# Performance work log

Measured on AMD Instinct MI355X. Metric: run time of the kernel, lower is better.

Reference implementation:

```python
import jax, jax.numpy as jnp
import numpy as np

GRID = 32          # latent grid points per dim
N_OUT = 16384      # output query points
BATCH = 2
C = 256            # projection_channels (latent hidden width)
D = 3              # gno_coord_dim
OUT_CH = 4         # out_channels
RADIUS = 0.045     # gno_radius


def _radius_neighbors(x, y, r):
    """Radius ball search: for each query x_i find all y_j with ||x_i-y_j||<=r.
    Returns (nb_index, out_index) edge lists, sorted by query (CSR order)."""
    r2 = np.float32(r * r)
    nb_idx, out_idx = [], []
    for s in range(0, x.shape[0], 512):  # chunk to bound memory
        d2 = ((x[s:s + 512, None, :] - y[None, :, :]) ** 2).sum(-1)
        oi, yi = np.nonzero(d2 <= r2)
        out_idx.append((oi + s).astype(np.int32))
        nb_idx.append(yi.astype(np.int32))
    return np.concatenate(nb_idx), np.concatenate(out_idx)


def setup_inputs() -> dict:
    key = jax.random.key(0)
    ks = jax.random.split(key, 8)
    # latent queries: regular grid on [0,1]^3
    g = np.linspace(0.0, 1.0, GRID, dtype=np.float32)
    gx, gy, gz = np.meshgrid(g, g, g, indexing="ij")
    grid = np.stack([gx, gy, gz], axis=-1)               # (G,G,G,3)
    latent_queries = jnp.asarray(grid[None])             # (1,G,G,G,3)
    output_queries = jax.random.uniform(ks[0], (1, N_OUT, D), dtype=jnp.float32)
    nb_idx, out_idx = _radius_neighbors(np.asarray(output_queries[0]),
                                        grid.reshape(-1, D), RADIUS)
    latent_embed = jax.random.normal(ks[1], (BATCH, GRID, GRID, GRID, C), dtype=jnp.float32)

    def lin(k, fi, fo):
        kw, kb = jax.random.split(k)
        W = jax.random.normal(kw, (fi, fo), dtype=jnp.float32) / np.sqrt(fi).astype(np.float32)
        b = jax.random.normal(kb, (fo,), dtype=jnp.float32) * 0.01
        return W, b

    W1, b1 = lin(ks[2], 2 * D, 512)
    W2, b2 = lin(ks[3], 512, 256)
    W3, b3 = lin(ks[4], 256, C)
    Wp, bp = lin(ks[5], C, OUT_CH)
    return {"latent_embed": latent_embed, "latent_queries": latent_queries,
            "output_queries": output_queries,
            "nb_index": jnp.asarray(nb_idx), "out_index": jnp.asarray(out_idx),
            "W1": W1, "b1": b1, "W2": W2, "b2": b2, "W3": W3, "b3": b3,
            "Wp": Wp, "bp": bp}


def reference(latent_embed, latent_queries, output_queries, nb_index, out_index,
              W1, b1, W2, b2, W3, b3, Wp, bp):
    y = latent_queries[0].reshape(-1, latent_queries.shape[-1])   # (n_in, d) grid coords
    x = output_queries[0]                                         # (n_out, d)
    n_out = x.shape[0]
    b = latent_embed.shape[0]
    f_y = latent_embed.reshape(b, -1, latent_embed.shape[-1])     # (b, n_in, c)

    # per-edge kernel MLP on concat(y_j, x_i) -- 'linear' transform type
    agg = jnp.concatenate([y[nb_index], x[out_index]], axis=-1)   # (E, 2d)
    h = jax.nn.gelu(agg @ W1 + b1, approximate=False)             # (E, 512)
    h = jax.nn.gelu(h @ W2 + b2, approximate=False)               # (E, 256)
    k = h @ W3 + b3                                               # (E, c) kernel values

    # k(x_i, y_j) * f(y_j), then mean-reduce over each neighborhood
    msg = k[None, :, :] * f_y[:, nb_index, :]                     # (b, E, c)
    sums = jax.vmap(lambda m: jax.ops.segment_sum(m, out_index, num_segments=n_out))(msg)
    cnt = jax.ops.segment_sum(jnp.ones(nb_index.shape[0], dtype=k.dtype),
                              out_index, num_segments=n_out)
    mean = sums / jnp.maximum(cnt, 1.0)[None, :, None]            # (b, n_out, c)

    # pointwise projection (single Linear, no nonlinearity)
    return mean @ Wp + bp                                         # (b, n_out, out_ch)
```

## Files before the change

kernel.cpp:

```cpp
#include <hip/hip_runtime.h>
#include <math.h>

#define NGRID 32768
#define NOUT  16384
#define CCH   256
#define H1DIM 512
#define TE    64
#define NTHR  512

typedef _Float16 f16x8 __attribute__((ext_vector_type(8)));
typedef float    f32x16 __attribute__((ext_vector_type(16)));

#define WAITVM1() asm volatile("s_waitcnt vmcnt(1)" ::: "memory")
#define WAITVM0() asm volatile("s_waitcnt vmcnt(0)" ::: "memory")
#define LGKM0_SB() do { asm volatile("s_waitcnt lgkmcnt(0)" ::: "memory"); \
                        __builtin_amdgcn_sched_barrier(0); } while (0)

typedef const __attribute__((address_space(1))) unsigned int* gas1_t;
typedef __attribute__((address_space(3))) unsigned int* las3_t;

__device__ __forceinline__ void stage16(const void* g, void* l) {
    __builtin_amdgcn_global_load_lds((gas1_t)g, (las3_t)l, 16, 0, 0);
}

__device__ __forceinline__ unsigned short f32_to_f16_bits(float v) {
    _Float16 h = (_Float16)v;
    return __builtin_bit_cast(unsigned short, h);
}

__device__ __forceinline__ float gelu_fast(float x) {
    float ax = fabsf(x) * 0.70710678118654752f;
    float t  = __builtin_amdgcn_rcpf(fmaf(0.3275911f, ax, 1.0f));
    float p  = fmaf(fmaf(fmaf(fmaf(1.061405429f, t, -1.453152027f), t, 1.421413741f), t,
                         -0.284496736f), t, 0.254829592f) * t;
    float e  = __expf(-ax * ax);
    float er = fmaf(-p, e, 1.0f);
    er = (x >= 0.0f) ? er : -er;
    return 0.5f * x * (1.0f + er);
}

__global__ __launch_bounds__(256) void gino_pack_kernel(
    const float* __restrict__ W2, const float* __restrict__ W3,
    unsigned short* __restrict__ W2F, unsigned short* __restrict__ W3F)
{
    int idx = blockIdx.x * 256 + threadIdx.x;
    if (idx < 32 * 8 * 64) {
        int l = idx & 63, g = (idx >> 6) & 7, ks = idx >> 9;
        int ch = g * 32 + (l & 31);
        int k0 = ks * 16 + (l >> 5) * 8;
        unsigned int u[4];
        #pragma unroll
        for (int p = 0; p < 4; ++p) {
            unsigned int lo = f32_to_f16_bits(W2[(k0 + 2 * p) * CCH + ch]);
            unsigned int hh = f32_to_f16_bits(W2[(k0 + 2 * p + 1) * CCH + ch]);
            u[p] = lo | (hh << 16);
        }
        *(uint4*)(W2F + idx * 8) = make_uint4(u[0], u[1], u[2], u[3]);
    } else if (idx < 32 * 8 * 64 + 16 * 8 * 64) {
        int i2 = idx - 32 * 8 * 64;
        int l = i2 & 63, g = (i2 >> 6) & 7, ks = i2 >> 9;
        int ch = g * 32 + (l & 31);
        int k0 = ks * 16 + (l >> 5) * 8;
        unsigned int u[4];
        #pragma unroll
        for (int p = 0; p < 4; ++p) {
            unsigned int lo = f32_to_f16_bits(W3[(k0 + 2 * p) * CCH + ch]);
            unsigned int hh = f32_to_f16_bits(W3[(k0 + 2 * p + 1) * CCH + ch]);
            u[p] = lo | (hh << 16);
        }
        *(uint4*)(W3F + i2 * 8) = make_uint4(u[0], u[1], u[2], u[3]);
    }
}

__global__ __launch_bounds__(NTHR, 4) void gino_edge_kernel(
    const float* __restrict__ latent_embed,
    const float* __restrict__ latent_queries,
    const float* __restrict__ output_queries,
    const int*   __restrict__ nb_index,
    const int*   __restrict__ out_index,
    const float* __restrict__ W1, const float* __restrict__ b1,
    const float* __restrict__ b2, const float* __restrict__ b3,
    const unsigned short* __restrict__ W2F,
    const unsigned short* __restrict__ W3F,
    const float* __restrict__ Wp,
    float* __restrict__ sums, float* __restrict__ cnt, int E)
{
    __shared__ __align__(16) unsigned char s_h1[TE * 256];
    __shared__ __align__(16) unsigned char s_h2[TE * 512];
    __shared__ __align__(16) unsigned char s_ab[8 * 2048];
    __shared__ float s_agg[TE][8];
    __shared__ float s_pm[TE][8];
    __shared__ int s_nb[TE], s_oi[TE], s_valid[TE];

    const int tid = threadIdx.x;
    const int e0  = blockIdx.x * TE;

    ((float*)s_pm)[tid] = 0.0f;
    if (tid < TE) {
        int e     = e0 + tid;
        int valid = (e < E) ? 1 : 0;
        int ec    = valid ? e : (E - 1);
        int nb    = nb_index[ec];
        int oi    = out_index[ec];
        s_nb[tid] = nb; s_oi[tid] = oi; s_valid[tid] = valid;
        s_agg[tid][0] = latent_queries[nb * 3 + 0];
        s_agg[tid][1] = latent_queries[nb * 3 + 1];
        s_agg[tid][2] = latent_queries[nb * 3 + 2];
        s_agg[tid][3] = output_queries[oi * 3 + 0];
        s_agg[tid][4] = output_queries[oi * 3 + 1];
        s_agg[tid][5] = output_queries[oi * 3 + 2];
        if (valid) atomicAdd(&cnt[oi], 1.0f);
    }
    __syncthreads();

    const int l  = tid & 63;
    const int w  = tid >> 6;
    const int le = l & 31;
    const int hi = l >> 5;
    const unsigned bsw1 = (unsigned)(le & 15) << 4;
    const unsigned bsw2 = (unsigned)(le & 31) << 4;
    unsigned char* abw = s_ab + w * 2048;

    f32x16 acc0 = {}, acc1 = {};

    #pragma unroll
    for (int c = 0; c < 4; ++c) {
        const unsigned short* gw = W2F + (size_t)(c * 8) * 4096 + w * 512 + l * 8;
        stage16(gw, abw);
        stage16(gw + 4096, abw + 1024);

        {
            const int col = c * 128 + l * 2;
            float w0[6], w1v[6];
            #pragma unroll
            for (int i = 0; i < 6; ++i) {
                float2 t2 = *(const float2*)(W1 + i * H1DIM + col);
                w0[i] = t2.x; w1v[i] = t2.y;
            }
            float2 bb = *(const float2*)(b1 + col);
            #pragma unroll
            for (int ee = 0; ee < 8; ++ee) {
                int e = w * 8 + ee;
                float v0 = bb.x, v1 = bb.y;
                #pragma unroll
                for (int i = 0; i < 6; ++i) {
                    float a = s_agg[e][i];
                    v0 = fmaf(a, w0[i], v0);
                    v1 = fmaf(a, w1v[i], v1);
                }
                unsigned u = (unsigned)f32_to_f16_bits(gelu_fast(v0)) |
                             ((unsigned)f32_to_f16_bits(gelu_fast(v1)) << 16);
                *(unsigned*)(s_h1 + e * 256 + (((unsigned)(l * 4)) ^ (((unsigned)(e & 15)) << 4))) = u;
            }
        }
        __syncthreads();

        #pragma unroll
        for (int ks = 0; ks < 8; ++ks) {
            if (ks < 7) WAITVM1(); else WAITVM0();
            f16x8 a  = *(const f16x8*)(abw + (ks & 1) * 1024 + l * 16);
            f16x8 b0 = *(const f16x8*)(s_h1 + le * 256 +
                           (((unsigned)(ks * 32 + hi * 16)) ^ bsw1));
            f16x8 b1f = *(const f16x8*)(s_h1 + (32 + le) * 256 +
                           (((unsigned)(ks * 32 + hi * 16)) ^ bsw1));
            LGKM0_SB();
            if (ks < 6) stage16(gw + (size_t)(ks + 2) * 4096, abw + (ks & 1) * 1024);
            acc0 = __builtin_amdgcn_mfma_f32_32x32x16_f16(a, b0,  acc0, 0, 0, 0);
            acc1 = __builtin_amdgcn_mfma_f32_32x32x16_f16(a, b1f, acc1, 0, 0, 0);
        }
        __syncthreads();
    }

    const unsigned short* gw3 = W3F + w * 512 + l * 8;
    stage16(gw3, abw);
    stage16(gw3 + 4096, abw + 1024);
    #pragma unroll
    for (int t = 0; t < 2; ++t) {
        int erow = t * 32 + le;
        unsigned esw = (unsigned)(erow & 31) << 4;
        #pragma unroll
        for (int q = 0; q < 4; ++q) {
            int ch0 = w * 32 + q * 8 + hi * 4;
            float4 bb = *(const float4*)(b2 + ch0);
            float v0 = (t ? acc1[q * 4 + 0] : acc0[q * 4 + 0]) + bb.x;
            float v1 = (t ? acc1[q * 4 + 1] : acc0[q * 4 + 1]) + bb.y;
            float v2 = (t ? acc1[q * 4 + 2] : acc0[q * 4 + 2]) + bb.z;
            float v3 = (t ? acc1[q * 4 + 3] : acc0[q * 4 + 3]) + bb.w;
            unsigned int u0 = f32_to_f16_bits(gelu_fast(v0)) |
                              ((unsigned)f32_to_f16_bits(gelu_fast(v1)) << 16);
            unsigned int u1 = f32_to_f16_bits(gelu_fast(v2)) |
                              ((unsigned)f32_to_f16_bits(gelu_fast(v3)) << 16);
            *(uint2*)(s_h2 + erow * 512 + (((unsigned)(ch0 * 2)) ^ esw)) = make_uint2(u0, u1);
        }
    }
    __syncthreads();

    f32x16 kc0 = {}, kc1 = {};
    #pragma unroll
    for (int ks = 0; ks < 16; ++ks) {
        if (ks < 15) WAITVM1(); else WAITVM0();
        f16x8 a  = *(const f16x8*)(abw + (ks & 1) * 1024 + l * 16);
        f16x8 b0 = *(const f16x8*)(s_h2 + le * 512 +
                       (((unsigned)(ks * 32 + hi * 16)) ^ bsw2));
        f16x8 b1f = *(const f16x8*)(s_h2 + (32 + le) * 512 +
                       (((unsigned)(ks * 32 + hi * 16)) ^ bsw2));
        LGKM0_SB();
        if (ks < 14) stage16(gw3 + (size_t)(ks + 2) * 4096, abw + (ks & 1) * 1024);
        kc0 = __builtin_amdgcn_mfma_f32_32x32x16_f16(a, b0,  kc0, 0, 0, 0);
        kc1 = __builtin_amdgcn_mfma_f32_32x32x16_f16(a, b1f, kc1, 0, 0, 0);
    }

    #pragma unroll
    for (int t = 0; t < 2; ++t) {
        int e  = t * 32 + le;
        int nb = s_nb[e];
        const float* fb0 = latent_embed + (size_t)nb * CCH;
        const float* fb1 = latent_embed + ((size_t)NGRID + nb) * CCH;
        float pm[8] = {0.f, 0.f, 0.f, 0.f, 0.f, 0.f, 0.f, 0.f};
        #pragma unroll
        for (int q = 0; q < 4; ++q) {
            int ch0 = w * 32 + q * 8 + hi * 4;
            float4 bb = *(const float4*)(b3 + ch0);
            float kv0 = (t ? kc1[q * 4 + 0] : kc0[q * 4 + 0]) + bb.x;
            float kv1 = (t ? kc1[q * 4 + 1] : kc0[q * 4 + 1]) + bb.y;
            float kv2 = (t ? kc1[q * 4 + 2] : kc0[q * 4 + 2]) + bb.z;
            float kv3 = (t ? kc1[q * 4 + 3] : kc0[q * 4 + 3]) + bb.w;
            float4 f0 = *(const float4*)(fb0 + ch0);
            float4 f1 = *(const float4*)(fb1 + ch0);
            float4 wp0 = *(const float4*)(Wp + (ch0 + 0) * 4);
            float4 wp1 = *(const float4*)(Wp + (ch0 + 1) * 4);
            float4 wp2 = *(const float4*)(Wp + (ch0 + 2) * 4);
            float4 wp3 = *(const float4*)(Wp + (ch0 + 3) * 4);
            float t0 = kv0 * f0.x, t1 = kv1 * f0.y, t2v = kv2 * f0.z, t3 = kv3 * f0.w;
            pm[0] = fmaf(t0, wp0.x, fmaf(t1, wp1.x, fmaf(t2v, wp2.x, fmaf(t3, wp3.x, pm[0]))));
            pm[1] = fmaf(t0, wp0.y, fmaf(t1, wp1.y, fmaf(t2v, wp2.y, fmaf(t3, wp3.y, pm[1]))));
            pm[2] = fmaf(t0, wp0.z, fmaf(t1, wp1.z, fmaf(t2v, wp2.z, fmaf(t3, wp3.z, pm[2]))));
            pm[3] = fmaf(t0, wp0.w, fmaf(t1, wp1.w, fmaf(t2v, wp2.w, fmaf(t3, wp3.w, pm[3]))));
            float s0 = kv0 * f1.x, s1 = kv1 * f1.y, s2 = kv2 * f1.z, s3 = kv3 * f1.w;
            pm[4] = fmaf(s0, wp0.x, fmaf(s1, wp1.x, fmaf(s2, wp2.x, fmaf(s3, wp3.x, pm[4]))));
            pm[5] = fmaf(s0, wp0.y, fmaf(s1, wp1.y, fmaf(s2, wp2.y, fmaf(s3, wp3.y, pm[5]))));
            pm[6] = fmaf(s0, wp0.z, fmaf(s1, wp1.z, fmaf(s2, wp2.z, fmaf(s3, wp3.z, pm[6]))));
            pm[7] = fmaf(s0, wp0.w, fmaf(s1, wp1.w, fmaf(s2, wp2.w, fmaf(s3, wp3.w, pm[7]))));
        }
        #pragma unroll
        for (int v = 0; v < 8; ++v) pm[v] += __shfl_xor(pm[v], 32);
        if (hi == 0) {
            #pragma unroll
            for (int v = 0; v < 8; ++v) atomicAdd(&s_pm[e][v], pm[v]);
        }
    }
    __syncthreads();

    {
        int el = tid >> 3;
        int v  = tid & 7;
        if (s_valid[el]) {
            int b  = v >> 2;
            int oc = v & 3;
            atomicAdd(&sums[((size_t)b * NOUT + s_oi[el]) * 4 + oc], s_pm[el][v]);
        }
    }
}

__global__ __launch_bounds__(256) void gino_finalize_kernel(
    const float* __restrict__ sums,
    const float* __restrict__ cnt,
    const float* __restrict__ bp,
    float* __restrict__ out)
{
    int idx = blockIdx.x * 256 + threadIdx.x;
    if (idx >= 2 * NOUT * 4) return;
    int oc = idx & 3;
    int i  = (idx >> 2) & (NOUT - 1);
    float c = fmaxf(cnt[i], 1.0f);
    out[idx] = sums[idx] / c + bp[oc];
}

extern "C" void kernel_launch(void* const* d_in, const int* in_sizes, int n_in,
                              void* d_out, int out_size, void* d_ws, size_t ws_size,
                              hipStream_t stream) {
    const float* latent_embed   = (const float*)d_in[0];
    const float* latent_queries = (const float*)d_in[1];
    const float* output_queries = (const float*)d_in[2];
    const int*   nb_index       = (const int*)d_in[3];
    const int*   out_index      = (const int*)d_in[4];
    const float* W1 = (const float*)d_in[5];
    const float* b1 = (const float*)d_in[6];
    const float* W2 = (const float*)d_in[7];
    const float* b2 = (const float*)d_in[8];
    const float* W3 = (const float*)d_in[9];
    const float* b3 = (const float*)d_in[10];
    const float* Wp = (const float*)d_in[11];
    const float* bp = (const float*)d_in[12];

    const int E = in_sizes[3];

    float* sums = (float*)d_ws;
    float* cnt  = sums + 2 * NOUT * 4;
    unsigned short* W2F = (unsigned short*)(cnt + NOUT);
    unsigned short* W3F = W2F + 32 * 8 * 64 * 8;

    hipMemsetAsync(d_ws, 0, (size_t)(2 * NOUT * 4 + NOUT) * sizeof(float), stream);

    gino_pack_kernel<<<(32 * 8 * 64 + 16 * 8 * 64 + 255) / 256, 256, 0, stream>>>(
        W2, W3, W2F, W3F);

    int nblk = (E + TE - 1) / TE;
    gino_edge_kernel<<<nblk, NTHR, 0, stream>>>(
        latent_embed, latent_queries, output_queries, nb_index, out_index,
        W1, b1, b2, b3, W2F, W3F, Wp, sums, cnt, E);

    gino_finalize_kernel<<<(2 * NOUT * 4 + 255) / 256, 256, 0, stream>>>(
        sums, cnt, bp, (float*)d_out);
}
```

Before: 267.0 us.

## Load MFMA weight fragments directly into registers instead of LDS double-buffer

Replaces the global_load_lds double-buffered staging of W2/W3 fragments with direct register loads of all k-step fragments issued up front. This removes the LDS round trip, the manual vmcnt/lgkmcnt waits and the sched barriers, and frees 16 KB of shared memory per block. In exchange it raises register pressure sharply (8 then 16 f16x8 vectors live at once) under a launch bound of 512 threads with 4 blocks per CU, which may cause spills or compiler-inserted waits. The loads are hoisted ahead of the layer-1 GELU work and the h2 epilogue so their latency overlaps that computation.

```diff
diff --git a/kernel.cpp b/kernel.cpp
--- a/kernel.cpp
+++ b/kernel.cpp
@@ -10,18 +10,6 @@
 
 typedef _Float16 f16x8 __attribute__((ext_vector_type(8)));
 typedef float    f32x16 __attribute__((ext_vector_type(16)));
-
-#define WAITVM1() asm volatile("s_waitcnt vmcnt(1)" ::: "memory")
-#define WAITVM0() asm volatile("s_waitcnt vmcnt(0)" ::: "memory")
-#define LGKM0_SB() do { asm volatile("s_waitcnt lgkmcnt(0)" ::: "memory"); \
-                        __builtin_amdgcn_sched_barrier(0); } while (0)
-
-typedef const __attribute__((address_space(1))) unsigned int* gas1_t;
-typedef __attribute__((address_space(3))) unsigned int* las3_t;
-
-__device__ __forceinline__ void stage16(const void* g, void* l) {
-    __builtin_amdgcn_global_load_lds((gas1_t)g, (las3_t)l, 16, 0, 0);
-}
 
 __device__ __forceinline__ unsigned short f32_to_f16_bits(float v) {
     _Float16 h = (_Float16)v;
@@ -87,7 +75,6 @@
 {
     __shared__ __align__(16) unsigned char s_h1[TE * 256];
     __shared__ __align__(16) unsigned char s_h2[TE * 512];
-    __shared__ __align__(16) unsigned char s_ab[8 * 2048];
     __shared__ float s_agg[TE][8];
     __shared__ float s_pm[TE][8];
     __shared__ int s_nb[TE], s_oi[TE], s_valid[TE];
@@ -119,15 +106,17 @@
     const int hi = l >> 5;
     const unsigned bsw1 = (unsigned)(le & 15) << 4;
     const unsigned bsw2 = (unsigned)(le & 31) << 4;
-    unsigned char* abw = s_ab + w * 2048;
 
     f32x16 acc0 = {}, acc1 = {};
 
     #pragma unroll
     for (int c = 0; c < 4; ++c) {
         const unsigned short* gw = W2F + (size_t)(c * 8) * 4096 + w * 512 + l * 8;
-        stage16(gw, abw);
-        stage16(gw + 4096, abw + 1024);
+        f16x8 a[8];
+        #pragma unroll
+        for (int ks = 0; ks < 8; ++ks)
+            a[ks] = *(const f16x8*)(gw + (size_t)ks * 4096);
+        __builtin_amdgcn_sched_barrier(0);
 
         {
             const int col = c * 128 + l * 2;
@@ -144,9 +133,9 @@
                 float v0 = bb.x, v1 = bb.y;
                 #pragma unroll
                 for (int i = 0; i < 6; ++i) {
-                    float a = s_agg[e][i];
-                    v0 = fmaf(a, w0[i], v0);
-                    v1 = fmaf(a, w1v[i], v1);
+                    float av = s_agg[e][i];
+                    v0 = fmaf(av, w0[i], v0);
+                    v1 = fmaf(av, w1v[i], v1);
                 }
                 unsigned u = (unsigned)f32_to_f16_bits(gelu_fast(v0)) |
                              ((unsigned)f32_to_f16_bits(gelu_fast(v1)) << 16);
@@ -157,23 +146,23 @@
 
         #pragma unroll
         for (int ks = 0; ks < 8; ++ks) {
-            if (ks < 7) WAITVM1(); else WAITVM0();
-            f16x8 a  = *(const f16x8*)(abw + (ks & 1) * 1024 + l * 16);
             f16x8 b0 = *(const f16x8*)(s_h1 + le * 256 +
                            (((unsigned)(ks * 32 + hi * 16)) ^ bsw1));
             f16x8 b1f = *(const f16x8*)(s_h1 + (32 + le) * 256 +
                            (((unsigned)(ks * 32 + hi * 16)) ^ bsw1));
-            LGKM0_SB();
-            if (ks < 6) stage16(gw + (size_t)(ks + 2) * 4096, abw + (ks & 1) * 1024);
-            acc0 = __builtin_amdgcn_mfma_f32_32x32x16_f16(a, b0,  acc0, 0, 0, 0);
-            acc1 = __builtin_amdgcn_mfma_f32_32x32x16_f16(a, b1f, acc1, 0, 0, 0);
+            acc0 = __builtin_amdgcn_mfma_f32_32x32x16_f16(a[ks], b0,  acc0, 0, 0, 0);
+            acc1 = __builtin_amdgcn_mfma_f32_32x32x16_f16(a[ks], b1f, acc1, 0, 0, 0);
         }
         __syncthreads();
     }
 
     const unsigned short* gw3 = W3F + w * 512 + l * 8;
-    stage16(gw3, abw);
-    stage16(gw3 + 4096, abw + 1024);
+    f16x8 a3[16];
+    #pragma unroll
+    for (int ks = 0; ks < 16; ++ks)
+        a3[ks] = *(const f16x8*)(gw3 + (size_t)ks * 4096);
+    __builtin_amdgcn_sched_barrier(0);
+
     #pragma unroll
     for (int t = 0; t < 2; ++t) {
         int erow = t * 32 + le;
@@ -198,16 +187,12 @@
     f32x16 kc0 = {}, kc1 = {};
     #pragma unroll
     for (int ks = 0; ks < 16; ++ks) {
-        if (ks < 15) WAITVM1(); else WAITVM0();
-        f16x8 a  = *(const f16x8*)(abw + (ks & 1) * 1024 + l * 16);
         f16x8 b0 = *(const f16x8*)(s_h2 + le * 512 +
                        (((unsigned)(ks * 32 + hi * 16)) ^ bsw2));
         f16x8 b1f = *(const f16x8*)(s_h2 + (32 + le) * 512 +
                        (((unsigned)(ks * 32 + hi * 16)) ^ bsw2));
-        LGKM0_SB();
-        if (ks < 14) stage16(gw3 + (size_t)(ks + 2) * 4096, abw + (ks & 1) * 1024);
-        kc0 = __builtin_amdgcn_mfma_f32_32x32x16_f16(a, b0,  kc0, 0, 0, 0);
-        kc1 = __builtin_amdgcn_mfma_f32_32x32x16_f16(a, b1f, kc1, 0, 0, 0);
+        kc0 = __builtin_amdgcn_mfma_f32_32x32x16_f16(a3[ks], b0,  kc0, 0, 0, 0);
+        kc1 = __builtin_amdgcn_mfma_f32_32x32x16_f16(a3[ks], b1f, kc1, 0, 0, 0);
     }
 
     #pragma unroll
```

Result: no change. 262.1 us (-1.8%).
